# Performance work log

Measured on AMD Instinct MI355X. Metric: run time of the kernel, lower is better.

## Reference

```python
import jax, jax.numpy as jnp
import numpy as np

B, NPG, HID, HEADS, L = 8, 512, 128, 8, 4
N = B * NPG
E = 16384
EDIM = HID // 4  # edge_dim = hidden_dim // 4 = 32


def _ln(x, g, b):
    m = x.mean(-1, keepdims=True)
    v = ((x - m) ** 2).mean(-1, keepdims=True)
    return (x - m) / jnp.sqrt(v + 1e-5) * g + b


def setup_inputs() -> dict:
    key = jax.random.key(0)
    ks = jax.random.split(key, 24)
    s = 0.05
    epg = E // B
    base = jnp.repeat(jnp.arange(B) * NPG, epg)
    src = base + jax.random.randint(ks[0], (E,), 0, NPG)
    dst = base + jax.random.randint(ks[1], (E,), 0, NPG)
    d = {
        'x': jax.random.randint(ks[2], (N, 1), 0, 100),
        'edge_index': jnp.stack([src, dst]),
        'edge_attr': jax.random.normal(ks[3], (E, 1), jnp.float32),
        'batch': jnp.repeat(jnp.arange(B), NPG),
        'atom_emb': jax.random.normal(ks[4], (100, HID)) * s,
        'edge_w': jax.random.normal(ks[5], (1, EDIM)) * s,
        'edge_b': jnp.zeros((EDIM,)),
        'wq': jax.random.normal(ks[6], (L, HID, HEADS * HID)) * s,
        'bq': jnp.zeros((L, HEADS * HID)),
        'wk': jax.random.normal(ks[7], (L, HID, HEADS * HID)) * s,
        'bk': jnp.zeros((L, HEADS * HID)),
        'wv': jax.random.normal(ks[8], (L, HID, HEADS * HID)) * s,
        'bv': jnp.zeros((L, HEADS * HID)),
        'we': jax.random.normal(ks[9], (L, EDIM, HEADS * HID)) * s,
        'wskip': jax.random.normal(ks[10], (L, HID, HID)) * s,
        'bskip': jnp.zeros((L, HID)),
        'ln_g': jnp.ones((L, HID)),
        'ln_b': jnp.zeros((L, HID)),
        'mha_in_w': jax.random.normal(ks[11], (HID, 3 * HID)) * s,
        'mha_in_b': jnp.zeros((3 * HID,)),
        'mha_out_w': jax.random.normal(ks[12], (HID, HID)) * s,
        'mha_out_b': jnp.zeros((HID,)),
        'w1': jax.random.normal(ks[13], (HID, HID)) * s,
        'b1': jnp.zeros((HID,)),
        'w2': jax.random.normal(ks[14], (HID, HID // 2)) * s,
        'b2': jnp.zeros((HID // 2,)),
        'w3': jax.random.normal(ks[15], (HID // 2, 3)) * s,
        'b3': jnp.zeros((3,)),
    }
    return d


def reference(x, edge_index, edge_attr, batch, atom_emb, edge_w, edge_b,
              wq, bq, wk, bk, wv, bv, we, wskip, bskip, ln_g, ln_b,
              mha_in_w, mha_in_b, mha_out_w, mha_out_b, w1, b1, w2, b2, w3, b3):
    src, dst = edge_index[0], edge_index[1]
    h = atom_emb[x[:, 0]]                       # [N, HID]
    e = edge_attr @ edge_w + edge_b             # [E, EDIM]
    scale = 1.0 / jnp.sqrt(jnp.float32(HID))    # per-head channel dim = HID
    for i in range(L):
        res = h
        q = (h @ wq[i] + bq[i]).reshape(N, HEADS, HID)
        k = (h @ wk[i] + bk[i]).reshape(N, HEADS, HID)
        v = (h @ wv[i] + bv[i]).reshape(N, HEADS, HID)
        ee = (e @ we[i]).reshape(E, HEADS, HID)
        kj = k[src] + ee                        # [E, HEADS, HID]
        vj = v[src] + ee
        logits = jnp.einsum('ehd,ehd->eh', q[dst], kj) * scale
        m = jax.ops.segment_max(logits, dst, num_segments=N)
        a = jnp.exp(logits - m[dst])
        z = jax.ops.segment_sum(a, dst, num_segments=N)
        a = a / (z[dst] + 1e-16)                # edge softmax per target node
        agg = jax.ops.segment_sum(a[:, :, None] * vj, dst, num_segments=N)
        out = agg.mean(axis=1) + h @ wskip[i] + bskip[i]  # concat=False + root skip
        h = jax.nn.gelu(_ln(out + res, ln_g[i], ln_b[i]), approximate=False)
    # equal-size graphs: ragged->padded conversion is a plain reshape, no padding
    p = h.reshape(B, NPG, HID)
    qkv = p @ mha_in_w + mha_in_b               # [B, n, 3*HID]
    hd = HID // HEADS
    q, k, v = [t.reshape(B, NPG, HEADS, hd).transpose(0, 2, 1, 3)
               for t in jnp.split(qkv, 3, axis=-1)]
    att = jax.nn.softmax(jnp.einsum('bhqd,bhkd->bhqk', q, k) / jnp.sqrt(jnp.float32(hd)), axis=-1)
    o = jnp.einsum('bhqk,bhkd->bhqd', att, v).transpose(0, 2, 1, 3).reshape(B, NPG, HID)
    o = (o @ mha_out_w + mha_out_b).reshape(N, HID)
    y = jax.nn.gelu(o @ w1 + b1, approximate=False)
    y = jax.nn.gelu(y @ w2 + b2, approximate=False)
    return y @ w3 + b3                          # [N, 3]
```

## Files before the change

### kernel.cpp

```cpp
#include <hip/hip_runtime.h>
#include <hip/hip_bf16.h>
#include <math.h>

#define NN 4096
#define NE 16384
#define NLAYERS 4

#define WT_STRIDE 442368

typedef __attribute__((ext_vector_type(8))) short bf16x8;
typedef __attribute__((ext_vector_type(4))) float floatx4;

__device__ __forceinline__ float gelu_f(float x) {
  return 0.5f * x * (1.0f + erff(x * 0.70710678118654752440f));
}

__device__ __forceinline__ void bsplit(float a, unsigned short& hi, unsigned short& lo) {
  __hip_bfloat16 h16 = __float2bfloat16(a);
  hi = *(unsigned short*)&h16;
  const float r = a - __bfloat162float(h16);
  __hip_bfloat16 l16 = __float2bfloat16(r);
  lo = *(unsigned short*)&l16;
}

union F16U { float4 v4[4]; float f[16]; };

__global__ void k_init(const int* __restrict__ x, const float* __restrict__ atom_emb,
                       const float* __restrict__ edge_attr, const float* __restrict__ edge_w,
                       const float* __restrict__ edge_b, float* __restrict__ h,
                       float* __restrict__ ef, int* __restrict__ counts,
                       unsigned short* __restrict__ hhi, unsigned short* __restrict__ hlo) {
  const int idx = blockIdx.x * 256 + threadIdx.x;
  const float hv = atom_emb[x[idx >> 7] * 128 + (idx & 127)];
  h[idx] = hv;
  bsplit(hv, hhi[idx], hlo[idx]);
  ef[idx] = edge_attr[idx >> 5] * edge_w[idx & 31] + edge_b[idx & 31];
  if (idx < NN) counts[idx] = 0;
}

__global__ void k_hist(const int* __restrict__ eidx, int* __restrict__ counts) {
  const int e = blockIdx.x * 256 + threadIdx.x;
  if (e < NE) atomicAdd(&counts[eidx[NE + e]], 1);
}

__global__ void k_scan(const int* __restrict__ counts, int* __restrict__ offs,
                       int* __restrict__ heads) {
  __shared__ int tmp[1024];
  const int t = threadIdx.x;
  const int c0 = counts[t*4], c1 = counts[t*4+1], c2 = counts[t*4+2], c3 = counts[t*4+3];
  const int s = c0 + c1 + c2 + c3;
  tmp[t] = s; __syncthreads();
  for (int off = 1; off < 1024; off <<= 1) {
    int v = (t >= off) ? tmp[t - off] : 0;
    __syncthreads();
    tmp[t] += v;
    __syncthreads();
  }
  int base = tmp[t] - s;
  offs[t*4]   = base;                heads[t*4]   = base;
  offs[t*4+1] = base + c0;           heads[t*4+1] = base + c0;
  offs[t*4+2] = base + c0 + c1;      heads[t*4+2] = base + c0 + c1;
  offs[t*4+3] = base + c0 + c1 + c2; heads[t*4+3] = base + c0 + c1 + c2;
  if (t == 1023) offs[NN] = tmp[1023];
}

__global__ void k_scatter(const int* __restrict__ eidx, int* __restrict__ heads,
                          int* __restrict__ elist) {
  const int e = blockIdx.x * 256 + threadIdx.x;
  if (e < NE) {
    int p = atomicAdd(&heads[eidx[NE + e]], 1);
    elist[p] = e;
  }
}

__global__ __launch_bounds__(256) void k_wcvt(
    const float* __restrict__ wq, const float* __restrict__ wk,
    const float* __restrict__ wv, const float* __restrict__ wsk,
    unsigned short* __restrict__ wthi, unsigned short* __restrict__ wtlo) {
  const int z = blockIdx.z;
  const int layer = z >> 2, mat = z & 3;
  int NC; const float* W; int woff;
  if (mat == 0)      { NC = 1024; W = wq  + (size_t)layer * 131072; woff = 0; }
  else if (mat == 1) { NC = 1024; W = wk  + (size_t)layer * 131072; woff = 131072; }
  else if (mat == 2) { NC = 1024; W = wv  + (size_t)layer * 131072; woff = 262144; }
  else               { NC = 128;  W = wsk + (size_t)layer * 16384;  woff = 393216; }
  const int c0 = blockIdx.x * 64;
  if (c0 >= NC) return;
  const int k0 = blockIdx.y * 64;
  __shared__ unsigned short th[64][65], tl[64][65];
  const int t = threadIdx.x;
  for (int i = t; i < 4096; i += 256) {
    const int kk = i >> 6, c = i & 63;
    bsplit(W[(size_t)(k0 + kk) * NC + c0 + c], th[kk][c], tl[kk][c]);
  }
  __syncthreads();
  unsigned short* oh = wthi + (size_t)layer * WT_STRIDE + woff;
  unsigned short* ol = wtlo + (size_t)layer * WT_STRIDE + woff;
  for (int i = t; i < 4096; i += 256) {
    const int n = i >> 6, k = i & 63;
    oh[(size_t)(c0 + n) * 128 + k0 + k] = th[k][n];
    ol[(size_t)(c0 + n) * 128 + k0 + k] = tl[k][n];
  }
}

__global__ __launch_bounds__(256) void k_wqe(
    const float* __restrict__ wq, const float* __restrict__ bq,
    const float* __restrict__ we, unsigned short* __restrict__ wthi,
    unsigned short* __restrict__ wtlo, float* __restrict__ bqe) {
  const int layer = blockIdx.x >> 3, hh = blockIdx.x & 7;
  const float* wq_l = wq + (size_t)layer * 131072;
  const float* we_l = we + (size_t)layer * 32768;
  const float* bq_l = bq + (size_t)layer * 1024;
  __shared__ float wqS[128][132];
  __shared__ float weS[32][132];
  const int t = threadIdx.x;
  for (int i = t; i < 4096; i += 256) {
    const int d = i >> 5, dd4 = (i & 31) << 2;
    *(float4*)&wqS[d][dd4] = *(const float4*)&wq_l[(size_t)d * 1024 + hh * 128 + dd4];
  }
  for (int i = t; i < 1024; i += 256) {
    const int c = i >> 5, dd4 = (i & 31) << 2;
    *(float4*)&weS[c][dd4] = *(const float4*)&we_l[(size_t)c * 1024 + hh * 128 + dd4];
  }
  __syncthreads();
  const int d = t & 127, cg = t >> 7;
  float acc[16];
  #pragma unroll
  for (int cc = 0; cc < 16; cc++) acc[cc] = 0.f;
  for (int dd = 0; dd < 128; dd++) {
    const float a = wqS[d][dd];
    #pragma unroll
    for (int cc = 0; cc < 16; cc++)
      acc[cc] += a * weS[cg * 16 + cc][dd];
  }
  unsigned short* oh = wthi + (size_t)layer * WT_STRIDE + 409600;
  unsigned short* ol = wtlo + (size_t)layer * WT_STRIDE + 409600;
  #pragma unroll
  for (int cc = 0; cc < 16; cc++) {
    const int j = hh * 32 + cg * 16 + cc;
    unsigned short hi, lo;
    bsplit(acc[cc], hi, lo);
    oh[(size_t)j * 128 + d] = hi;
    ol[(size_t)j * 128 + d] = lo;
  }
  if (t < 32) {
    float s = 0.f;
    for (int dd = 0; dd < 128; dd++) s += bq_l[hh * 128 + dd] * weS[t][dd];
    bqe[layer * 256 + hh * 32 + t] = s;
  }
}

__global__ __launch_bounds__(256) void k_mfqkv(
    const unsigned short* __restrict__ hhi, const unsigned short* __restrict__ hlo,
    const unsigned short* __restrict__ wth, const unsigned short* __restrict__ wtl,
    const float* __restrict__ bq, const float* __restrict__ bk,
    const float* __restrict__ bv, const float* __restrict__ bsk,
    const float* __restrict__ bqe_l,
    float* __restrict__ qb, float* __restrict__ kb,
    float* __restrict__ vb, float* __restrict__ skb, float* __restrict__ qeb) {
  const int xb = blockIdx.x;
  int NC; const float* bias; float* C; int woff; int c0;
  if (xb < 16)      { NC = 1024; bias = bq;    C = qb;  woff = 0;      c0 = xb * 64; }
  else if (xb < 32) { NC = 1024; bias = bk;    C = kb;  woff = 131072; c0 = (xb-16) * 64; }
  else if (xb < 48) { NC = 1024; bias = bv;    C = vb;  woff = 262144; c0 = (xb-32) * 64; }
  else if (xb < 50) { NC = 128;  bias = bsk;   C = skb; woff = 393216; c0 = (xb-48) * 64; }
  else              { NC = 256;  bias = bqe_l; C = qeb; woff = 409600; c0 = (xb-50) * 64; }
  __shared__ unsigned short Ah[64][136], Al[64][136], Wh[64][136], Wl[64][136];
  const int t = threadIdx.x;
  const int n0 = blockIdx.y * 64;
  for (int i = t; i < 1024; i += 256) {
    const int r = i >> 4, c8 = (i & 15) << 3;
    *(uint4*)&Ah[r][c8] = *(const uint4*)&hhi[(size_t)(n0 + r) * 128 + c8];
    *(uint4*)&Al[r][c8] = *(const uint4*)&hlo[(size_t)(n0 + r) * 128 + c8];
    *(uint4*)&Wh[r][c8] = *(const uint4*)&wth[woff + (size_t)(c0 + r) * 128 + c8];
    *(uint4*)&Wl[r][c8] = *(const uint4*)&wtl[woff + (size_t)(c0 + r) * 128 + c8];
  }
  __syncthreads();
  const int w = t >> 6, l = t & 63;
  const int quad = l >> 4, lm = l & 15;
  floatx4 acc[4] = {{0.f,0.f,0.f,0.f},{0.f,0.f,0.f,0.f},{0.f,0.f,0.f,0.f},{0.f,0.f,0.f,0.f}};
  #pragma unroll
  for (int kc = 0; kc < 4; kc++) {
    const int ko = kc * 32 + quad * 8;
    const bf16x8 ah = *(const bf16x8*)&Ah[w * 16 + lm][ko];
    const bf16x8 al = *(const bf16x8*)&Al[w * 16 + lm][ko];
    #pragma unroll
    for (int ct = 0; ct < 4; ct++) {
      const bf16x8 bh = *(const bf16x8*)&Wh[ct * 16 + lm][ko];
      const bf16x8 bl = *(const bf16x8*)&Wl[ct * 16 + lm][ko];
      acc[ct] = __builtin_amdgcn_mfma_f32_16x16x32_bf16(ah, bh, acc[ct], 0, 0, 0);
      acc[ct] = __builtin_amdgcn_mfma_f32_16x16x32_bf16(ah, bl, acc[ct], 0, 0, 0);
      acc[ct] = __builtin_amdgcn_mfma_f32_16x16x32_bf16(al, bh, acc[ct], 0, 0, 0);
    }
  }
  #pragma unroll
  for (int ct = 0; ct < 4; ct++) {
    const int col = c0 + ct * 16 + lm;
    const float bb = bias[col];
    #pragma unroll
    for (int r = 0; r < 4; r++) {
      const int row = n0 + w * 16 + quad * 4 + r;
      C[(size_t)row * NC + col] = acc[ct][r] + bb;
    }
  }
}

__global__ __launch_bounds__(256) void k_gemm2(const float* __restrict__ A,
                                               const float* __restrict__ W,
                                               const float* __restrict__ bias,
                                               float* __restrict__ C, int NC, int gelu) {
  __shared__ float As[128][65];
  __shared__ float Ws[128][64];
  const int t = threadIdx.x;
  const int n0 = blockIdx.y * 64, c0 = blockIdx.x * 64;
  for (int i = t; i < 2048; i += 256) {
    const int r = i & 63, k4 = (i >> 6) << 2;
    const float4 a = *(const float4*)&A[(size_t)(n0 + r) * 128 + k4];
    As[k4+0][r] = a.x; As[k4+1][r] = a.y; As[k4+2][r] = a.z; As[k4+3][r] = a.w;
  }
  for (int i = t; i < 2048; i += 256) {
    const int kk = i >> 4, c4 = (i & 15) << 2;
    *(float4*)&Ws[kk][c4] = *(const float4*)&W[(size_t)kk * NC + c0 + c4];
  }
  __syncthreads();
  const int tr = (t >> 4) << 2;
  const int tc = (t & 15) << 2;
  float acc[4][4];
  #pragma unroll
  for (int i = 0; i < 4; i++)
    #pragma unroll
    for (int j = 0; j < 4; j++) acc[i][j] = 0.f;
  #pragma unroll 8
  for (int k = 0; k < 128; k++) {
    const float4 av = *(const float4*)&As[k][tr];
    const float4 wv = *(const float4*)&Ws[k][tc];
    acc[0][0] += av.x*wv.x; acc[0][1] += av.x*wv.y; acc[0][2] += av.x*wv.z; acc[0][3] += av.x*wv.w;
    acc[1][0] += av.y*wv.x; acc[1][1] += av.y*wv.y; acc[1][2] += av.y*wv.z; acc[1][3] += av.y*wv.w;
    acc[2][0] += av.z*wv.x; acc[2][1] += av.z*wv.y; acc[2][2] += av.z*wv.z; acc[2][3] += av.z*wv.w;
    acc[3][0] += av.w*wv.x; acc[3][1] += av.w*wv.y; acc[3][2] += av.w*wv.z; acc[3][3] += av.w*wv.w;
  }
  const float4 bb = *(const float4*)&bias[c0 + tc];
  #pragma unroll
  for (int i = 0; i < 4; i++) {
    float4 v;
    v.x = acc[i][0] + bb.x; v.y = acc[i][1] + bb.y;
    v.z = acc[i][2] + bb.z; v.w = acc[i][3] + bb.w;
    if (gelu) { v.x = gelu_f(v.x); v.y = gelu_f(v.y); v.z = gelu_f(v.z); v.w = gelu_f(v.w); }
    *(float4*)&C[(size_t)(n0 + tr + i) * NC + c0 + tc] = v;
  }
}

__global__ __launch_bounds__(256) void k_corrpost(
    const float* __restrict__ sbuf, const float* __restrict__ we_l,
    const float* __restrict__ accm, const float* __restrict__ skb,
    const float* __restrict__ lng, const float* __restrict__ lnb,
    float* __restrict__ h,
    unsigned short* __restrict__ hhi, unsigned short* __restrict__ hlo) {
  __shared__ float As[32][256];
  __shared__ float Ws[128][64];
  __shared__ float sC[32][129];
  const int t = threadIdx.x;
  const int n0 = blockIdx.x * 32;
  for (int i = t; i < 2048; i += 256) {
    const int r = i >> 6, c4 = (i & 63) << 2;
    *(float4*)&As[r][c4] = *(const float4*)&sbuf[(size_t)(n0 + r) * 256 + c4];
  }
  const int tx = t & 63, ty = t >> 6;
  float acc[2][8];
  #pragma unroll
  for (int cc = 0; cc < 2; cc++)
    #pragma unroll
    for (int j = 0; j < 8; j++) acc[cc][j] = 0.f;
  #pragma unroll
  for (int cc = 0; cc < 2; cc++) {
    const int c0 = cc * 64;
    for (int kc = 0; kc < 2; kc++) {
      __syncthreads();
      for (int i = t; i < 2048; i += 256) {
        const int kk = i >> 4, c4 = (i & 15) << 2;
        const int k = kc * 128 + kk;
        const int hh = k >> 5, c = k & 31;
        *(float4*)&Ws[kk][c4] = *(const float4*)&we_l[(size_t)c * 1024 + hh * 128 + c0 + c4];
      }
      __syncthreads();
      for (int kk = 0; kk < 128; kk += 4) {
        const float w0 = Ws[kk+0][tx];
        const float w1 = Ws[kk+1][tx];
        const float w2 = Ws[kk+2][tx];
        const float w3 = Ws[kk+3][tx];
        #pragma unroll
        for (int j = 0; j < 8; j++) {
          const float4 a = *(const float4*)&As[ty*8 + j][kc*128 + kk];
          acc[cc][j] += a.x*w0 + a.y*w1 + a.z*w2 + a.w*w3;
        }
      }
    }
  }
  #pragma unroll
  for (int j = 0; j < 8; j++) {
    sC[ty*8 + j][tx]      = acc[0][j];
    sC[ty*8 + j][64 + tx] = acc[1][j];
  }
  __syncthreads();
  const int w = t >> 6, lane = t & 63;
  const float g0c = lng[lane], g1c = lng[64 + lane];
  const float b0c = lnb[lane], b1c = lnb[64 + lane];
  for (int j = 0; j < 8; j++) {
    const int nn = w * 8 + j;
    const size_t o = (size_t)(n0 + nn) * 128;
    const float v0 = accm[o + lane]      + 0.125f * sC[nn][lane]      + skb[o + lane]      + h[o + lane];
    const float v1 = accm[o + 64 + lane] + 0.125f * sC[nn][64 + lane] + skb[o + 64 + lane] + h[o + 64 + lane];
    float s = v0 + v1;
    #pragma unroll
    for (int mask = 1; mask <= 32; mask <<= 1) s += __shfl_xor(s, mask);
    const float mean = s * (1.f / 128.f);
    const float d0 = v0 - mean, d1 = v1 - mean;
    float vs = d0*d0 + d1*d1;
    #pragma unroll
    for (int mask = 1; mask <= 32; mask <<= 1) vs += __shfl_xor(vs, mask);
    const float rstd = 1.f / sqrtf(vs * (1.f / 128.f) + 1e-5f);
    const float y0 = d0 * rstd * g0c + b0c;
    const float y1 = d1 * rstd * g1c + b1c;
    const float r0 = gelu_f(y0);
    const float r1 = gelu_f(y1);
    h[o + lane] = r0;
    h[o + 64 + lane] = r1;
    bsplit(r0, hhi[o + lane], hlo[o + lane]);
    bsplit(r1, hhi[o + 64 + lane], hlo[o + 64 + lane]);
  }
}

__global__ __launch_bounds__(256) void k_edge(const float* __restrict__ qb,
                                              const float* __restrict__ kb,
                                              const float* __restrict__ vb,
                                              const float* __restrict__ qe,
                                              const float* __restrict__ ef,
                                              const int* __restrict__ offs,
                                              const int* __restrict__ elist,
                                              const int* __restrict__ eidx,
                                              float* __restrict__ accm,
                                              float* __restrict__ sbuf) {
  const int wid = threadIdx.x >> 6;
  const int n = (blockIdx.x & 7) * 512 + (blockIdx.x >> 3) * 4 + wid;
  const int lane = threadIdx.x & 63;
  const int hh = lane >> 3, s8 = lane & 7;
  const int d0 = hh * 128 + s8 * 16;
  F16U qv;
  {
    const float4* qp = (const float4*)(qb + (size_t)n * 1024 + d0);
    #pragma unroll
    for (int i = 0; i < 4; i++) qv.v4[i] = qp[i];
  }
  const float4 qe4 = *(const float4*)(qe + (size_t)n * 256 + hh * 32 + s8 * 4);
  float m = -INFINITY, z = 0.f;
  float acc[16];
  #pragma unroll
  for (int i = 0; i < 16; i++) acc[i] = 0.f;
  float sx = 0.f, sy = 0.f, sz = 0.f, sw = 0.f;
  const int e0 = offs[n], e1 = offs[n + 1];
  for (int tt = e0; tt < e1; tt++) {
    const int e = elist[tt];
    const int src = eidx[e];
    F16U kv;
    {
      const float4* kp = (const float4*)(kb + (size_t)src * 1024 + d0);
      #pragma unroll
      for (int i = 0; i < 4; i++) kv.v4[i] = kp[i];
    }
    const float4 ef4 = *(const float4*)(ef + (size_t)e * 32 + s8 * 4);
    float p0 = qe4.x*ef4.x + qe4.y*ef4.y;
    float p1 = qe4.z*ef4.z + qe4.w*ef4.w;
    float p2 = 0.f, p3 = 0.f;
    #pragma unroll
    for (int i = 0; i < 4; i++) {
      p0 += qv.f[i]      * kv.f[i];
      p1 += qv.f[4 + i]  * kv.f[4 + i];
      p2 += qv.f[8 + i]  * kv.f[8 + i];
      p3 += qv.f[12 + i] * kv.f[12 + i];
    }
    float p = (p0 + p1) + (p2 + p3);
    p += __shfl_xor(p, 1);
    p += __shfl_xor(p, 2);
    p += __shfl_xor(p, 4);
    const float logit = p * 0.08838834764831845f;
    if (logit > m + 8.f) {
      const float f = __expf(m - logit);
      z *= f; sx *= f; sy *= f; sz *= f; sw *= f;
      #pragma unroll
      for (int i = 0; i < 16; i++) acc[i] *= f;
      m = logit;
    }
    const float w = __expf(logit - m);
    z += w;
    F16U vv;
    {
      const float4* vp = (const float4*)(vb + (size_t)src * 1024 + d0);
      #pragma unroll
      for (int i = 0; i < 4; i++) vv.v4[i] = vp[i];
    }
    #pragma unroll
    for (int i = 0; i < 16; i++) acc[i] += w * vv.f[i];
    sx += w * ef4.x; sy += w * ef4.y;
    sz += w * ef4.z; sw += w * ef4.w;
  }
  const float inv = 1.f / (z + 1e-16f);
  *(float4*)(sbuf + (size_t)n * 256 + hh * 32 + s8 * 4) =
      make_float4(sx * inv, sy * inv, sz * inv, sw * inv);
  F16U ov;
  #pragma unroll
  for (int i = 0; i < 16; i++) ov.f[i] = acc[i] * inv;
  #pragma unroll
  for (int mask = 8; mask <= 32; mask <<= 1)
    #pragma unroll
    for (int i = 0; i < 16; i++) ov.f[i] += __shfl_xor(ov.f[i], mask);
  if (hh == 0) {
    #pragma unroll
    for (int i = 0; i < 16; i++) ov.f[i] *= 0.125f;
    float4* ap = (float4*)(accm + (size_t)n * 128 + s8 * 16);
    #pragma unroll
    for (int i = 0; i < 4; i++) ap[i] = ov.v4[i];
  }
}

__global__ __launch_bounds__(256) void k_attn2b(const float* __restrict__ qkvm,
                                                float* __restrict__ pm,
                                                float* __restrict__ pz,
                                                float* __restrict__ pacc) {
  __shared__ float ks2[64][16];
  __shared__ float vs2[64][16];
  const int ksp = blockIdx.x, qt = blockIdx.y, bh = blockIdx.z;
  const int b = bh >> 3, hh = bh & 7;
  const int t = threadIdx.x;
  const size_t rbase = (size_t)(b * 512 + ksp * 64);
  {
    const int j = t >> 2, d4 = (t & 3) << 2;
    const size_t ro = (rbase + j) * 384 + hh * 16 + d4;
    *(float4*)&ks2[j][d4] = *(const float4*)&qkvm[ro + 128];
    *(float4*)&vs2[j][d4] = *(const float4*)&qkvm[ro + 256];
  }
  __syncthreads();
  const int qrow = qt * 256 + t;
  const int nq = b * 512 + qrow;
  F16U qv;
  {
    const float4* qp = (const float4*)(qkvm + (size_t)nq * 384 + hh * 16);
    #pragma unroll
    for (int i = 0; i < 4; i++) qv.v4[i] = qp[i];
  }
  float m = -INFINITY, z = 0.f;
  float acc[16];
  #pragma unroll
  for (int i = 0; i < 16; i++) acc[i] = 0.f;
  for (int j = 0; j < 64; j += 2) {
    F16U k0, k1, v0, v1;
    {
      const float4* p0 = (const float4*)ks2[j];
      const float4* p1 = (const float4*)ks2[j + 1];
      const float4* q0 = (const float4*)vs2[j];
      const float4* q1 = (const float4*)vs2[j + 1];
      #pragma unroll
      for (int i = 0; i < 4; i++) {
        k0.v4[i] = p0[i]; k1.v4[i] = p1[i];
        v0.v4[i] = q0[i]; v1.v4[i] = q1[i];
      }
    }
    float a0 = 0.f, a1 = 0.f, a2 = 0.f, a3 = 0.f;
    float b0 = 0.f, b1 = 0.f, b2 = 0.f, b3 = 0.f;
    #pragma unroll
    for (int i = 0; i < 4; i++) {
      a0 += qv.f[i]      * k0.f[i];
      a1 += qv.f[4 + i]  * k0.f[4 + i];
      a2 += qv.f[8 + i]  * k0.f[8 + i];
      a3 += qv.f[12 + i] * k0.f[12 + i];
      b0 += qv.f[i]      * k1.f[i];
      b1 += qv.f[4 + i]  * k1.f[4 + i];
      b2 += qv.f[8 + i]  * k1.f[8 + i];
      b3 += qv.f[12 + i] * k1.f[12 + i];
    }
    const float sa = ((a0 + a1) + (a2 + a3)) * 0.25f;
    const float sb = ((b0 + b1) + (b2 + b3)) * 0.25f;
    const float smax = fmaxf(sa, sb);
    if (smax > m + 8.f) {
      const float f = __expf(m - smax);
      z *= f;
      #pragma unroll
      for (int i = 0; i < 16; i++) acc[i] *= f;
      m = smax;
    }
    const float wa = __expf(sa - m);
    const float wb = __expf(sb - m);
    z += wa + wb;
    #pragma unroll
    for (int i = 0; i < 16; i++)
      acc[i] += wa * v0.f[i] + wb * v1.f[i];
  }
  const int p = (bh * 512 + qrow) * 8 + ksp;
  pm[p] = m; pz[p] = z;
  float4* pp = (float4*)&pacc[(size_t)p * 16];
  F16U ov;
  #pragma unroll
  for (int i = 0; i < 16; i++) ov.f[i] = acc[i];
  #pragma unroll
  for (int i = 0; i < 4; i++) pp[i] = ov.v4[i];
}

__global__ void k_amerge(const float* __restrict__ pm, const float* __restrict__ pz,
                         const float* __restrict__ pacc, float* __restrict__ ob) {
  const int idx = blockIdx.x * 256 + threadIdx.x;
  if (idx >= 32768) return;
  const int bh = idx >> 9, qrow = idx & 511;
  const int b = bh >> 3, hh = bh & 7;
  float ms = pm[idx*8];
  #pragma unroll
  for (int s = 1; s < 8; s++) ms = fmaxf(ms, pm[idx*8+s]);
  float wgt[8];
  float z = 0.f;
  #pragma unroll
  for (int s = 0; s < 8; s++) {
    wgt[s] = __expf(pm[idx*8+s] - ms);
    z += pz[idx*8+s] * wgt[s];
  }
  const float inv = 1.f / z;
  float* op = &ob[(size_t)(b * 512 + qrow) * 128 + hh * 16];
  #pragma unroll
  for (int d = 0; d < 16; d++) {
    float o = 0.f;
    #pragma unroll
    for (int s = 0; s < 8; s++)
      o += pacc[(size_t)(idx*8+s) * 16 + d] * wgt[s];
    op[d] = o * inv;
  }
}

__global__ void k_final(const float* __restrict__ y2, const float* __restrict__ w3,
                        const float* __restrict__ b3, float* __restrict__ out) {
  const int idx = blockIdx.x * 256 + threadIdx.x;
  if (idx >= NN * 3) return;
  const int n = idx / 3, j = idx % 3;
  float s = b3[j];
  const float* yp = y2 + (size_t)n * 64;
  #pragma unroll
  for (int c = 0; c < 64; c++) s += yp[c] * w3[c * 3 + j];
  out[idx] = s;
}

extern "C" void kernel_launch(void* const* d_in, const int* in_sizes, int n_in,
                              void* d_out, int out_size, void* d_ws, size_t ws_size,
                              hipStream_t stream) {
  const int*   x         = (const int*)d_in[0];
  const int*   eidx      = (const int*)d_in[1];
  const float* edge_attr = (const float*)d_in[2];
  const float* atom_emb  = (const float*)d_in[4];
  const float* edge_w    = (const float*)d_in[5];
  const float* edge_b    = (const float*)d_in[6];
  const float* wq        = (const float*)d_in[7];
  const float* bq        = (const float*)d_in[8];
  const float* wk        = (const float*)d_in[9];
  const float* bk        = (const float*)d_in[10];
  const float* wv        = (const float*)d_in[11];
  const float* bv        = (const float*)d_in[12];
  const float* we        = (const float*)d_in[13];
  const float* wskip     = (const float*)d_in[14];
  const float* bskip     = (const float*)d_in[15];
  const float* ln_g      = (const float*)d_in[16];
  const float* ln_b      = (const float*)d_in[17];
  const float* mha_in_w  = (const float*)d_in[18];
  const float* mha_in_b  = (const float*)d_in[19];
  const float* mha_out_w = (const float*)d_in[20];
  const float* mha_out_b = (const float*)d_in[21];
  const float* w1        = (const float*)d_in[22];
  const float* b1        = (const float*)d_in[23];
  const float* w2        = (const float*)d_in[24];
  const float* b2        = (const float*)d_in[25];
  const float* w3        = (const float*)d_in[26];
  const float* b3        = (const float*)d_in[27];

  float* ws   = (float*)d_ws;
  float* h    = ws;
  float* ef   = h + 524288;
  float* qb   = ef + 524288;
  float* kb   = qb + 4194304;
  float* vb   = kb + 4194304;
  float* qe   = vb + 4194304;
  float* big  = qe + 1048576;
  float* accm = big;
  float* skb  = big + 1048576;
  unsigned short* hhi  = (unsigned short*)(big + 1572864);
  unsigned short* hlo  = hhi + 524288;
  unsigned short* wthi = hlo + 524288;
  unsigned short* wtlo = wthi + 1769472;
  float* sbuf = big + 4194304;
  float* qkvm = qb;
  float* pm   = sbuf;
  float* pz   = sbuf + 262144;
  float* pacc = big;
  float* ob   = kb;
  float* mo   = kb + 524288;
  float* y1   = kb + 1048576;
  float* y2   = kb + 1572864;
  int* counts = (int*)(sbuf + 1048576);
  int* offs   = counts + 4100;
  int* heads  = offs + 4100;
  int* elist  = heads + 4100;
  float* bqe  = (float*)(elist + 16384);

  k_init<<<2048, 256, 0, stream>>>(x, atom_emb, edge_attr, edge_w, edge_b, h, ef, counts,
                                   hhi, hlo);
  k_hist<<<64, 256, 0, stream>>>(eidx, counts);
  k_scan<<<1, 1024, 0, stream>>>(counts, offs, heads);
  k_scatter<<<64, 256, 0, stream>>>(eidx, heads, elist);
  k_wcvt<<<dim3(16, 2, 16), 256, 0, stream>>>(wq, wk, wv, wskip, wthi, wtlo);
  k_wqe<<<32, 256, 0, stream>>>(wq, bq, we, wthi, wtlo, bqe);

  for (int i = 0; i < NLAYERS; i++) {
    const float* bq_i  = bq + (size_t)i * 1024;
    const float* bk_i  = bk + (size_t)i * 1024;
    const float* bv_i  = bv + (size_t)i * 1024;
    const float* we_i  = we + (size_t)i * 32768;
    const float* bsk_i = bskip + (size_t)i * 128;
    const float* g_i   = ln_g + (size_t)i * 128;
    const float* b_i   = ln_b + (size_t)i * 128;
    const unsigned short* wth_i = wthi + (size_t)i * WT_STRIDE;
    const unsigned short* wtl_i = wtlo + (size_t)i * WT_STRIDE;

    k_mfqkv<<<dim3(54, 64), 256, 0, stream>>>(hhi, hlo, wth_i, wtl_i,
                                              bq_i, bk_i, bv_i, bsk_i, bqe + i * 256,
                                              qb, kb, vb, skb, qe);
    k_edge<<<1024, 256, 0, stream>>>(qb, kb, vb, qe, ef, offs, elist, eidx, accm, sbuf);
    k_corrpost<<<128, 256, 0, stream>>>(sbuf, we_i, accm, skb, g_i, b_i, h, hhi, hlo);
  }

  k_gemm2<<<dim3(6, 64), 256, 0, stream>>>(h, mha_in_w, mha_in_b, qkvm, 384, 0);
  k_attn2b<<<dim3(8, 2, 64), 256, 0, stream>>>(qkvm, pm, pz, pacc);
  k_amerge<<<128, 256, 0, stream>>>(pm, pz, pacc, ob);
  k_gemm2<<<dim3(2, 64), 256, 0, stream>>>(ob, mha_out_w, mha_out_b, mo, 128, 0);
  k_gemm2<<<dim3(2, 64), 256, 0, stream>>>(mo, w1, b1, y1, 128, 1);
  k_gemm2<<<dim3(1, 64), 256, 0, stream>>>(y1, w2, b2, y2, 64, 1);
  k_final<<<48, 256, 0, stream>>>(y2, w3, b3, (float*)d_out);
}
```

Measured before the change: 561.0 us.

## Restructure corrpost into small 8-node blocks with direct weight reads

```diff
diff --git a/kernel.cpp b/kernel.cpp
--- a/kernel.cpp
+++ b/kernel.cpp
@@ -256,77 +256,58 @@
     const float* __restrict__ lng, const float* __restrict__ lnb,
     float* __restrict__ h,
     unsigned short* __restrict__ hhi, unsigned short* __restrict__ hlo) {
-  __shared__ float As[32][256];
-  __shared__ float Ws[128][64];
-  __shared__ float sC[32][129];
+  __shared__ float Ss[8][256];
+  __shared__ float sC[8][128];
   const int t = threadIdx.x;
-  const int n0 = blockIdx.x * 32;
-  for (int i = t; i < 2048; i += 256) {
+  const int n0 = blockIdx.x * 8;
+  for (int i = t; i < 512; i += 256) {
     const int r = i >> 6, c4 = (i & 63) << 2;
-    *(float4*)&As[r][c4] = *(const float4*)&sbuf[(size_t)(n0 + r) * 256 + c4];
-  }
-  const int tx = t & 63, ty = t >> 6;
-  float acc[2][8];
-  #pragma unroll
-  for (int cc = 0; cc < 2; cc++)
-    #pragma unroll
-    for (int j = 0; j < 8; j++) acc[cc][j] = 0.f;
-  #pragma unroll
-  for (int cc = 0; cc < 2; cc++) {
-    const int c0 = cc * 64;
-    for (int kc = 0; kc < 2; kc++) {
-      __syncthreads();
-      for (int i = t; i < 2048; i += 256) {
-        const int kk = i >> 4, c4 = (i & 15) << 2;
-        const int k = kc * 128 + kk;
-        const int hh = k >> 5, c = k & 31;
-        *(float4*)&Ws[kk][c4] = *(const float4*)&we_l[(size_t)c * 1024 + hh * 128 + c0 + c4];
-      }
-      __syncthreads();
-      for (int kk = 0; kk < 128; kk += 4) {
-        const float w0 = Ws[kk+0][tx];
-        const float w1 = Ws[kk+1][tx];
-        const float w2 = Ws[kk+2][tx];
-        const float w3 = Ws[kk+3][tx];
-        #pragma unroll
-        for (int j = 0; j < 8; j++) {
-          const float4 a = *(const float4*)&As[ty*8 + j][kc*128 + kk];
-          acc[cc][j] += a.x*w0 + a.y*w1 + a.z*w2 + a.w*w3;
-        }
-      }
-    }
-  }
-  #pragma unroll
-  for (int j = 0; j < 8; j++) {
-    sC[ty*8 + j][tx]      = acc[0][j];
-    sC[ty*8 + j][64 + tx] = acc[1][j];
+    *(float4*)&Ss[r][c4] = *(const float4*)&sbuf[(size_t)(n0 + r) * 256 + c4];
   }
   __syncthreads();
-  const int w = t >> 6, lane = t & 63;
-  const float g0c = lng[lane], g1c = lng[64 + lane];
-  const float b0c = lnb[lane], b1c = lnb[64 + lane];
-  for (int j = 0; j < 8; j++) {
-    const int nn = w * 8 + j;
-    const size_t o = (size_t)(n0 + nn) * 128;
-    const float v0 = accm[o + lane]      + 0.125f * sC[nn][lane]      + skb[o + lane]      + h[o + lane];
-    const float v1 = accm[o + 64 + lane] + 0.125f * sC[nn][64 + lane] + skb[o + 64 + lane] + h[o + 64 + lane];
-    float s = v0 + v1;
-    #pragma unroll
-    for (int mask = 1; mask <= 32; mask <<= 1) s += __shfl_xor(s, mask);
-    const float mean = s * (1.f / 128.f);
-    const float d0 = v0 - mean, d1 = v1 - mean;
-    float vs = d0*d0 + d1*d1;
-    #pragma unroll
-    for (int mask = 1; mask <= 32; mask <<= 1) vs += __shfl_xor(vs, mask);
-    const float rstd = 1.f / sqrtf(vs * (1.f / 128.f) + 1e-5f);
-    const float y0 = d0 * rstd * g0c + b0c;
-    const float y1 = d1 * rstd * g1c + b1c;
-    const float r0 = gelu_f(y0);
-    const float r1 = gelu_f(y1);
-    h[o + lane] = r0;
-    h[o + 64 + lane] = r1;
-    bsplit(r0, hhi[o + lane], hlo[o + lane]);
-    bsplit(r1, hhi[o + 64 + lane], hlo[o + 64 + lane]);
+  const int col = t & 127, half = t >> 7;
+  float acc[4] = {0.f, 0.f, 0.f, 0.f};
+  const float* wp = we_l + col;
+  #pragma unroll
+  for (int hh = 0; hh < 8; hh++) {
+    #pragma unroll 4
+    for (int c = 0; c < 32; c++) {
+      const float wv = wp[(size_t)c * 1024 + hh * 128];
+      const int k = hh * 32 + c;
+      #pragma unroll
+      for (int j = 0; j < 4; j++)
+        acc[j] += Ss[half * 4 + j][k] * wv;
+    }
+  }
+  #pragma unroll
+  for (int j = 0; j < 4; j++) {
+    const int nn = half * 4 + j;
+    const size_t o = (size_t)(n0 + nn) * 128 + col;
+    sC[nn][col] = accm[o] + 0.125f * acc[j] + skb[o] + h[o];
+  }
+  __syncthreads();
+  const int g = t >> 5, l = t & 31;
+  float v[4];
+  #pragma unroll
+  for (int jj = 0; jj < 4; jj++) v[jj] = sC[g][l + 32 * jj];
+  float s = (v[0] + v[1]) + (v[2] + v[3]);
+  #pragma unroll
+  for (int mask = 1; mask <= 16; mask <<= 1) s += __shfl_xor(s, mask);
+  const float mean = s * (1.f / 128.f);
+  float q = 0.f;
+  #pragma unroll
+  for (int jj = 0; jj < 4; jj++) { const float d = v[jj] - mean; q += d * d; }
+  #pragma unroll
+  for (int mask = 1; mask <= 16; mask <<= 1) q += __shfl_xor(q, mask);
+  const float rstd = 1.f / sqrtf(q * (1.f / 128.f) + 1e-5f);
+  #pragma unroll
+  for (int jj = 0; jj < 4; jj++) {
+    const int c2 = l + 32 * jj;
+    const float y = (v[jj] - mean) * rstd * lng[c2] + lnb[c2];
+    const float r = gelu_f(y);
+    const size_t o = (size_t)(n0 + g) * 128 + c2;
+    h[o] = r;
+    bsplit(r, hhi[o], hlo[o]);
   }
 }
 
@@ -627,7 +608,7 @@
                                               bq_i, bk_i, bv_i, bsk_i, bqe + i * 256,
                                               qb, kb, vb, skb, qe);
     k_edge<<<1024, 256, 0, stream>>>(qb, kb, vb, qe, ef, offs, elist, eidx, accm, sbuf);
-    k_corrpost<<<128, 256, 0, stream>>>(sbuf, we_i, accm, skb, g_i, b_i, h, hhi, hlo);
+    k_corrpost<<<512, 256, 0, stream>>>(sbuf, we_i, accm, skb, g_i, b_i, h, hhi, hlo);
   }
 
   k_gemm2<<<dim3(6, 64), 256, 0, stream>>>(h, mha_in_w, mha_in_b, qkvm, 384, 0);
```

After: 529.6 us. 1.06x faster.
